# Kernel optimization log

Measured on AMD Instinct MI355X. Metric: run time of the kernel, lower is better.

The kernel has to match this reference:

```python
import jax, jax.numpy as jnp
import numpy as np

RES = 64
FDIM = 32
NMOD = 3
HID = 64
NCLS = 4
NFREQ = 6
IN_DIM = FDIM * NMOD + 3 * (2 * NFREQ + 1)  # 135


def trilinear_sample(grid, pts):
    """Torch F.grid_sample(mode='bilinear', padding_mode='zeros', align_corners=True).
    grid: [C, D, H, W]; pts: [M, 3] with (x, y, z) in [-1, 1], x indexes W, y->H, z->D.
    Returns [M, C]."""
    C, D, H, W = grid.shape
    x, y, z = pts[:, 0], pts[:, 1], pts[:, 2]
    ix = (x + 1.0) * 0.5 * (W - 1)
    iy = (y + 1.0) * 0.5 * (H - 1)
    iz = (z + 1.0) * 0.5 * (D - 1)
    ix0 = jnp.floor(ix); iy0 = jnp.floor(iy); iz0 = jnp.floor(iz)
    fx = ix - ix0; fy = iy - iy0; fz = iz - iz0
    ix0i = ix0.astype(jnp.int32); ix1i = ix0i + 1
    iy0i = iy0.astype(jnp.int32); iy1i = iy0i + 1
    iz0i = iz0.astype(jnp.int32); iz1i = iz0i + 1

    def corner(zc, yc, xc, w):
        valid = ((zc >= 0) & (zc < D) & (yc >= 0) & (yc < H) & (xc >= 0) & (xc < W))
        zcc = jnp.clip(zc, 0, D - 1)
        ycc = jnp.clip(yc, 0, H - 1)
        xcc = jnp.clip(xc, 0, W - 1)
        v = grid[:, zcc, ycc, xcc]  # [C, M]
        return v * (w * valid.astype(grid.dtype))

    wx0 = 1.0 - fx; wx1 = fx
    wy0 = 1.0 - fy; wy1 = fy
    wz0 = 1.0 - fz; wz1 = fz
    out = (corner(iz0i, iy0i, ix0i, wz0 * wy0 * wx0)
           + corner(iz0i, iy0i, ix1i, wz0 * wy0 * wx1)
           + corner(iz0i, iy1i, ix0i, wz0 * wy1 * wx0)
           + corner(iz0i, iy1i, ix1i, wz0 * wy1 * wx1)
           + corner(iz1i, iy0i, ix0i, wz1 * wy0 * wx0)
           + corner(iz1i, iy0i, ix1i, wz1 * wy0 * wx1)
           + corner(iz1i, iy1i, ix0i, wz1 * wy1 * wx0)
           + corner(iz1i, iy1i, ix1i, wz1 * wy1 * wx1))
    return out.T  # [M, C]


def positional_encoding(x):
    # gamma(p) = [p, sin(2^0 pi p), cos(2^0 pi p), ..., sin(2^(L-1) pi p), cos(2^(L-1) pi p)]
    freqs = 2.0 ** jnp.arange(NFREQ, dtype=x.dtype)  # [L]
    enc = [x]
    for i in range(NFREQ):
        a = jnp.pi * freqs[i] * x
        enc.append(jnp.sin(a))
        enc.append(jnp.cos(a))
    return jnp.concatenate(enc, axis=-1)  # [..., 3*(2L+1)]


def setup_inputs() -> dict:
    key = jax.random.key(0)
    ks = jax.random.split(key, 8)
    B, N = 4, 131072
    points = jax.random.uniform(ks[0], (B, N, 3), jnp.float32, -1.0, 1.0)
    grids = jax.random.normal(ks[1], (NMOD, FDIM, RES, RES, RES), jnp.float32) * 0.1

    def xavier(k, fan_in, fan_out):
        a = np.sqrt(6.0 / (fan_in + fan_out))
        return jax.random.uniform(k, (fan_in, fan_out), jnp.float32, -a, a)

    W0 = xavier(ks[2], IN_DIM, HID); b0 = jnp.zeros((HID,), jnp.float32)
    W1 = xavier(ks[3], HID, HID); b1 = jnp.zeros((HID,), jnp.float32)
    W2 = xavier(ks[4], HID, 1 + NCLS); b2 = jnp.zeros((1 + NCLS,), jnp.float32)
    return {"points": points, "grids": grids, "W0": W0, "b0": b0,
            "W1": W1, "b1": b1, "W2": W2, "b2": b2}


def reference(points, grids, W0, b0, W1, b1, W2, b2):
    B, N, _ = points.shape
    pts = points.reshape(B * N, 3)
    # fuse all 3 modalities: cat along feature dim, modality-major order
    feats = jax.vmap(lambda g: trilinear_sample(g, pts))(grids)  # [3, M, C]
    fused = jnp.transpose(feats, (1, 0, 2)).reshape(B * N, NMOD * FDIM)
    pe = positional_encoding(pts)  # [M, 39]
    h = jnp.concatenate([fused, pe], axis=-1)  # [M, 135]
    h = jax.nn.relu(h @ W0 + b0)
    h = jax.nn.relu(h @ W1 + b1)
    o = h @ W2 + b2  # [M, 1 + num_classes]
    density = jax.nn.softplus(o[..., 0]).reshape(B, N)
    seg_logits = o[..., 1:].reshape(B, N, NCLS)
    return density, seg_logits
```

## Files before the change

### kernel.cpp

```cpp
#include <hip/hip_runtime.h>
#include <hip/hip_bf16.h>
#include <hip/hip_fp16.h>
#include <math.h>

#define RESX 64
#define NVOX (RESX * RESX * RESX)
#define FDIM 32
#define NMOD 3
#define HID 64
#define NCLS 4
#define NFREQ 6
#define INDIM 135
#define TPB 64
#define XK 168
#define XSTR 65
#define MSTRIDE_B (NVOX * FDIM * 2)
#define NCELL 4096
#define NREP 16
#define NBT (NVOX / 128)
#define TRB (NMOD * NBT)
#define HISTB 2048
#define PACKB 15

typedef _Float16 f16x8 __attribute__((ext_vector_type(8)));
typedef float    f32x4 __attribute__((ext_vector_type(4)));

static __device__ __forceinline__ __half2 u2h(unsigned int u) {
    return __builtin_bit_cast(__half2, u);
}
static __device__ __forceinline__ unsigned int h2u(__half2 h) {
    return __builtin_bit_cast(unsigned int, h);
}

static __device__ __forceinline__ int cell_of(float px, float py, float pz) {
    int x0 = (int)floorf((px + 1.0f) * 0.5f * (RESX - 1));
    int y0 = (int)floorf((py + 1.0f) * 0.5f * (RESX - 1));
    int z0 = (int)floorf((pz + 1.0f) * 0.5f * (RESX - 1));
    x0 = min(max(x0, 0), RESX - 1);
    y0 = min(max(y0, 0), RESX - 1);
    z0 = min(max(z0, 0), RESX - 1);
    return ((z0 >> 2) << 8) | ((y0 >> 2) << 4) | (x0 >> 2);
}

#define W0PACK (5 * 4 * 64 * 8)
#define W1PACK (2 * 4 * 64 * 8)
#define W2PACK (2 * 64 * 8)

__global__ void pre_kernel(const float* __restrict__ g,
                           _Float16* __restrict__ gt,
                           const float* __restrict__ W0,
                           const float* __restrict__ W1,
                           const float* __restrict__ W2,
                           _Float16* __restrict__ wb,
                           const float* __restrict__ points,
                           unsigned int* __restrict__ hist, int M) {
    __shared__ float4 tile4[FDIM][33];
    const int bid = blockIdx.x;
    const int t   = threadIdx.x;
    if (bid < TRB) {
        const int m  = bid / NBT;
        const int v0 = (bid % NBT) * 128;
        const float4* g4 = reinterpret_cast<const float4*>(g);
#pragma unroll
        for (int k = 0; k < 4; ++k) {
            const int idx = k * 256 + t;
            const int c = idx >> 5, q = idx & 31;
            tile4[c][q] = g4[((size_t)(m * FDIM + c) * NVOX + v0) / 4 + q];
        }
        __syncthreads();
        uint4* gtu4 = reinterpret_cast<uint4*>(gt);
#pragma unroll
        for (int k = 0; k < 2; ++k) {
            const int idx = k * 256 + t;
            const int v = idx >> 2, q = idx & 3;
            const int vq = v >> 2, vr = v & 3;
            uint4 o;
            {
                const float a0 = reinterpret_cast<const float*>(&tile4[8 * q + 0][vq])[vr];
                const float a1 = reinterpret_cast<const float*>(&tile4[8 * q + 1][vq])[vr];
                const float a2 = reinterpret_cast<const float*>(&tile4[8 * q + 2][vq])[vr];
                const float a3 = reinterpret_cast<const float*>(&tile4[8 * q + 3][vq])[vr];
                const float a4 = reinterpret_cast<const float*>(&tile4[8 * q + 4][vq])[vr];
                const float a5 = reinterpret_cast<const float*>(&tile4[8 * q + 5][vq])[vr];
                const float a6 = reinterpret_cast<const float*>(&tile4[8 * q + 6][vq])[vr];
                const float a7 = reinterpret_cast<const float*>(&tile4[8 * q + 7][vq])[vr];
                o.x = h2u(__floats2half2_rn(a0, a1));
                o.y = h2u(__floats2half2_rn(a2, a3));
                o.z = h2u(__floats2half2_rn(a4, a5));
                o.w = h2u(__floats2half2_rn(a6, a7));
            }
            gtu4[(size_t)(m * NVOX + v0 + v) * 4 + q] = o;
        }
    } else if (bid < TRB + HISTB) {
        const int hb = bid - TRB;
        const int i  = hb * 256 + t;
        const int r  = hb & (NREP - 1);
        if (i < M) {
            const int c = cell_of(points[i * 3], points[i * 3 + 1], points[i * 3 + 2]);
            atomicAdd(&hist[r * NCELL + c], 1u);
        }
    } else {
        const int tt = (bid - TRB - HISTB) * 256 + t;
        const int NT = PACKB * 256;
        for (int idx = tt; idx < W0PACK; idx += NT) {
            const int j = idx & 7, l = (idx >> 3) & 63, nt = (idx >> 9) & 3, s = idx >> 11;
            const int k = 32 * s + (l >> 4) * 8 + j;
            const int o = 16 * nt + (l & 15);
            wb[idx] = (_Float16)((k < INDIM) ? W0[k * HID + o] : 0.0f);
        }
        for (int idx = tt; idx < W1PACK; idx += NT) {
            const int j = idx & 7, l = (idx >> 3) & 63, nt = (idx >> 9) & 3, s = idx >> 11;
            const int k = 32 * s + (l >> 4) * 8 + j;
            const int o = 16 * nt + (l & 15);
            wb[W0PACK + idx] = (_Float16)W1[k * HID + o];
        }
        for (int idx = tt; idx < W2PACK; idx += NT) {
            const int j = idx & 7, l = (idx >> 3) & 63, s = idx >> 9;
            const int k = 32 * s + (l >> 4) * 8 + j;
            const int o = l & 15;
            wb[W0PACK + W1PACK + idx] =
                (_Float16)((o < NCLS + 1) ? W2[k * (NCLS + 1) + o] : 0.0f);
        }
    }
}

__global__ void scan_rep_kernel(unsigned int* __restrict__ hist,
                                unsigned int* __restrict__ tot) {
    const int c = blockIdx.x * 256 + threadIdx.x;
    unsigned int run = 0;
#pragma unroll
    for (int r = 0; r < NREP; ++r) {
        const unsigned int v = hist[r * NCELL + c];
        hist[r * NCELL + c] = run;
        run += v;
    }
    tot[c] = run;
}

__global__ __launch_bounds__(1024) void scan_kernel(const unsigned int* __restrict__ tot,
                                                    unsigned int* __restrict__ cbase) {
    __shared__ unsigned int s[1024];
    const int t = threadIdx.x;
    unsigned int v[4];
#pragma unroll
    for (int j = 0; j < 4; ++j) v[j] = tot[4 * t + j];
    const unsigned int sum = v[0] + v[1] + v[2] + v[3];
    s[t] = sum;
    __syncthreads();
    for (int off = 1; off < 1024; off <<= 1) {
        const unsigned int x = (t >= off) ? s[t - off] : 0u;
        __syncthreads();
        s[t] += x;
        __syncthreads();
    }
    unsigned int excl = s[t] - sum;
#pragma unroll
    for (int j = 0; j < 4; ++j) { cbase[4 * t + j] = excl; excl += v[j]; }
}

__global__ void scatter_kernel(const float* __restrict__ points,
                               const unsigned int* __restrict__ cbase,
                               unsigned int* __restrict__ hist,
                               float4* __restrict__ pts4, int M) {
    const int i = blockIdx.x * 256 + threadIdx.x;
    if (i < M) {
        const float px = points[i * 3], py = points[i * 3 + 1], pz = points[i * 3 + 2];
        const int c = cell_of(px, py, pz);
        const int r = blockIdx.x & (NREP - 1);
        const unsigned int pos = cbase[c] + atomicAdd(&hist[r * NCELL + c], 1u);
        pts4[pos] = make_float4(px, py, pz, __int_as_float(i));
    }
}

template <bool SORT>
__global__ __launch_bounds__(256, 7) void fused_mfma_kernel(
    const float* __restrict__ points,
    const float4* __restrict__ pts4,
    const _Float16* __restrict__ gt,
    const _Float16* __restrict__ wb,
    const float* __restrict__ b0, const float* __restrict__ b1,
    const float* __restrict__ b2,
    float* __restrict__ density, float* __restrict__ seg) {
    __shared__ __align__(16) _Float16 Xs[TPB * XK];
    __shared__ __align__(16) uint4 PQ[TPB];
    const int tid = threadIdx.x;
    const int chunk = gridDim.x >> 3;
    const int sbid  = (blockIdx.x & 7) * chunk + (blockIdx.x >> 3);
    const int p0    = sbid * TPB;

    const int l = tid & 63;
    const int w = __builtin_amdgcn_readfirstlane(tid >> 6);

    float px = 0.0f, py = 0.0f, pz = 0.0f;
    int gp = 0;
    if (l < 16) {
        const int p  = w * 16 + l;
        const int sp = p0 + p;
        if (SORT) {
            const float4 q = pts4[sp];
            px = q.x; py = q.y; pz = q.z; gp = __float_as_int(q.w);
        } else {
            px = points[sp * 3]; py = points[sp * 3 + 1]; pz = points[sp * 3 + 2];
            gp = sp;
        }
        const float ix = (px + 1.0f) * 0.5f * (RESX - 1);
        const float iy = (py + 1.0f) * 0.5f * (RESX - 1);
        const float iz = (pz + 1.0f) * 0.5f * (RESX - 1);
        const float fx0 = floorf(ix), fy0 = floorf(iy), fz0 = floorf(iz);
        const float fx = ix - fx0, fy = iy - fy0, fz = iz - fz0;
        int x0 = (int)fx0, y0 = (int)fy0, z0 = (int)fz0;
        x0 = min(max(x0, 0), RESX - 1);
        y0 = min(max(y0, 0), RESX - 1);
        z0 = min(max(z0, 0), RESX - 1);
        const float wy0 = 1.0f - fy, wy1 = fy;
        const float wz0 = 1.0f - fz, wz1 = fz;
        const unsigned int b00 = (unsigned int)((z0 * 4096 + y0 * 64 + x0) * 64);
        unsigned int code =
            (unsigned int)__builtin_bit_cast(unsigned short, __float2half(fx));
        if (y0 < RESX - 1) code |= 0x10000u;
        if (z0 < RESX - 1) code |= 0x20000u;
        PQ[w * 16 + l] = make_uint4(b00, code,
                                    h2u(__floats2half2_rn(wz0 * wy0, wz0 * wy1)),
                                    h2u(__floats2half2_rn(wz1 * wy0, wz1 * wy1)));
    }

    {
        const int hw   = tid >> 5;
        const int lane = tid & 31;
        const int half = lane >> 4;
        const char* gbase = reinterpret_cast<const char*>(gt) + lane * 4;
        const __half2 one2 = __float2half2_rn(1.0f);
#pragma unroll
        for (int i = 0; i < 8; ++i) {
            const int p = hw * 8 + i;
            const uint4 q = PQ[p];
            const unsigned int dy = (q.y & 0x10000u) >> 4;
            const unsigned int dz = (q.y & 0x20000u) << 1;
            const unsigned int b00 = q.x;
            const unsigned int b01 = q.x + dy;
            const unsigned int b10 = q.x + dz;
            const unsigned int b11 = q.x + dy + dz;
            const __half fxh =
                __builtin_bit_cast(__half, (unsigned short)(q.y & 0xffffu));
            const __half2 fx2  = __half2half2(fxh);
            const __half2 wxh2 = half ? fx2 : __hsub2(one2, fx2);
            const __half2 wab = u2h(q.z);
            const __half2 wcd = u2h(q.w);
            const __half2 h00 = __hmul2(__low2half2(wab),  wxh2);
            const __half2 h01 = __hmul2(__high2half2(wab), wxh2);
            const __half2 h10 = __hmul2(__low2half2(wcd),  wxh2);
            const __half2 h11 = __hmul2(__high2half2(wcd), wxh2);
            unsigned int accu[NMOD];
#pragma unroll
            for (int m = 0; m < NMOD; ++m) {
                const char* gm = gbase + (size_t)m * MSTRIDE_B;
                const unsigned int u0 = *reinterpret_cast<const unsigned int*>(gm + b00);
                const unsigned int u1 = *reinterpret_cast<const unsigned int*>(gm + b01);
                const unsigned int u2 = *reinterpret_cast<const unsigned int*>(gm + b10);
                const unsigned int u3 = *reinterpret_cast<const unsigned int*>(gm + b11);
                __half2 a = __hmul2(h00, u2h(u0));
                a = __hfma2(h01, u2h(u1), a);
                a = __hfma2(h10, u2h(u2), a);
                a = __hfma2(h11, u2h(u3), a);
                accu[m] = h2u(a);
            }
#pragma unroll
            for (int m = 0; m < NMOD; ++m) {
                const unsigned int other = __shfl_xor(accu[m], 16, 64);
                const __half2 sum = __hadd2(u2h(accu[m]), u2h(other));
                if (lane < 16) {
                    *reinterpret_cast<unsigned int*>(
                        &Xs[p * XK + m * FDIM + 2 * (lane & 15)]) = h2u(sum);
                }
            }
        }
    }

    {
        const int src = l & 15;
        const float c0 = __shfl(px, src, 64);
        const float c1 = __shfl(py, src, 64);
        const float c2 = __shfl(pz, src, 64);
        const int pt  = w * 16 + src;
        const int gq2 = l >> 4;
        const float c3[3] = {c0, c1, c2};
        _Float16* xr = &Xs[pt * XK];
        if (gq2 == 3) {
            xr[96]  = (_Float16)c3[0];
            xr[97]  = (_Float16)c3[1];
            xr[98]  = (_Float16)c3[2];
            xr[135] = (_Float16)0.0f;
        }
        if (gq2 == 2) {
            unsigned int* xz = reinterpret_cast<unsigned int*>(&xr[136]);
#pragma unroll
            for (int k = 0; k < 12; ++k) xz[k] = 0u;
        }
        {
            const int f = gq2;
            const float hf = 0.5f * (float)(1 << f);
#pragma unroll
            for (int d = 0; d < 3; ++d) {
                const float r  = c3[d] * hf;
                const float rf = r - floorf(r);
                xr[99 + 6 * f + d]     = (_Float16)__builtin_amdgcn_sinf(rf);
                xr[99 + 6 * f + 3 + d] = (_Float16)__builtin_amdgcn_cosf(rf);
            }
        }
        if (gq2 < 2) {
            const int f = gq2 + 4;
            const float hf = 0.5f * (float)(1 << f);
#pragma unroll
            for (int d = 0; d < 3; ++d) {
                const float r  = c3[d] * hf;
                const float rf = r - floorf(r);
                xr[99 + 6 * f + d]     = (_Float16)__builtin_amdgcn_sinf(rf);
                xr[99 + 6 * f + 3 + d] = (_Float16)__builtin_amdgcn_cosf(rf);
            }
        }
    }

    const int col = l & 15;
    const int g   = l >> 4;

    f32x4 acc0[4];
#pragma unroll
    for (int nt = 0; nt < 4; ++nt) {
        const float bv = b0[nt * 16 + col];
        acc0[nt] = (f32x4){bv, bv, bv, bv};
    }
    {
        const _Float16* arow = &Xs[(w * 16 + col) * XK];
#pragma unroll
        for (int s = 0; s < 5; ++s) {
            const f16x8 af = *reinterpret_cast<const f16x8*>(arow + s * 32 + g * 8);
#pragma unroll
            for (int nt = 0; nt < 4; ++nt) {
                const f16x8 bfr = *reinterpret_cast<const f16x8*>(wb + (size_t)((s * 4 + nt) * 64 + l) * 8);
                acc0[nt] = __builtin_amdgcn_mfma_f32_16x16x32_f16(af, bfr, acc0[nt], 0, 0, 0);
            }
        }
    }
#pragma unroll
    for (int nt = 0; nt < 4; ++nt)
#pragma unroll
        for (int r = 0; r < 4; ++r) {
            Xs[(w * 16 + g * 4 + r) * XK + 96 + nt * 16 + col] =
                (_Float16)fmaxf(acc0[nt][r], 0.0f);
        }

    f32x4 acc1[4];
#pragma unroll
    for (int nt = 0; nt < 4; ++nt) {
        const float bv = b1[nt * 16 + col];
        acc1[nt] = (f32x4){bv, bv, bv, bv};
    }
    {
        const _Float16* arow = &Xs[(w * 16 + col) * XK + 96];
        const _Float16* wb1  = wb + W0PACK;
#pragma unroll
        for (int s = 0; s < 2; ++s) {
            const f16x8 af = *reinterpret_cast<const f16x8*>(arow + s * 32 + g * 8);
#pragma unroll
            for (int nt = 0; nt < 4; ++nt) {
                const f16x8 bfr = *reinterpret_cast<const f16x8*>(wb1 + (size_t)((s * 4 + nt) * 64 + l) * 8);
                acc1[nt] = __builtin_amdgcn_mfma_f32_16x16x32_f16(af, bfr, acc1[nt], 0, 0, 0);
            }
        }
    }
#pragma unroll
    for (int nt = 0; nt < 4; ++nt)
#pragma unroll
        for (int r = 0; r < 4; ++r) {
            Xs[(w * 16 + g * 4 + r) * XK + nt * 16 + col] =
                (_Float16)fmaxf(acc1[nt][r], 0.0f);
        }

    f32x4 acc2;
    {
        const float bv = (col < NCLS + 1) ? b2[col] : 0.0f;
        acc2 = (f32x4){bv, bv, bv, bv};
        const _Float16* arow = &Xs[(w * 16 + col) * XK];
        const _Float16* wb2  = wb + W0PACK + W1PACK;
#pragma unroll
        for (int s = 0; s < 2; ++s) {
            const f16x8 af  = *reinterpret_cast<const f16x8*>(arow + s * 32 + g * 8);
            const f16x8 bfr = *reinterpret_cast<const f16x8*>(wb2 + (size_t)(s * 64 + l) * 8);
            acc2 = __builtin_amdgcn_mfma_f32_16x16x32_f16(af, bfr, acc2, 0, 0, 0);
        }
    }
    if (col < NCLS + 1) {
        float* osr = reinterpret_cast<float*>(&Xs[0]);
#pragma unroll
        for (int r = 0; r < 4; ++r) {
            const int row = w * 16 + g * 4 + r;
            osr[(row * XK + 128) / 2 + col] = acc2[r];
        }
    }

    if (l < 16) {
        const int row = w * 16 + l;
        const float* osr = reinterpret_cast<const float*>(&Xs[0]) + (row * XK + 128) / 2;
        const float4 o0123 = *reinterpret_cast<const float4*>(osr);
        const float o4 = osr[4];
        const float e  = __builtin_amdgcn_exp2f(fabsf(o0123.x) * -1.44269504f);
        const float sp = fmaxf(o0123.x, 0.0f) + 0.69314718f * __builtin_amdgcn_logf(1.0f + e);
        density[gp] = sp;
        reinterpret_cast<float4*>(seg)[gp] = make_float4(o0123.y, o0123.z, o0123.w, o4);
    }
}

__global__ __launch_bounds__(256, 4) void fused_nerf_fallback(
    const float* __restrict__ points,
    const float* __restrict__ grids,
    const float* __restrict__ W0, const float* __restrict__ b0,
    const float* __restrict__ W1, const float* __restrict__ b1,
    const float* __restrict__ W2, const float* __restrict__ b2,
    float* __restrict__ density, float* __restrict__ seg) {
    __shared__ float xT[INDIM + 1][XSTR];
    const int tid = threadIdx.x;
    const int p0  = blockIdx.x * TPB;
    {
        const int hw   = tid >> 5;
        const int lane = tid & 31;
        for (int i = 0; i < TPB / 8; ++i) {
            const int p  = hw * (TPB / 8) + i;
            const int gp = p0 + p;
            const float px = points[gp * 3 + 0];
            const float py = points[gp * 3 + 1];
            const float pz = points[gp * 3 + 2];
            const float ix = (px + 1.0f) * 0.5f * (RESX - 1);
            const float iy = (py + 1.0f) * 0.5f * (RESX - 1);
            const float iz = (pz + 1.0f) * 0.5f * (RESX - 1);
            const float fx0 = floorf(ix), fy0 = floorf(iy), fz0 = floorf(iz);
            const float fx = ix - fx0, fy = iy - fy0, fz = iz - fz0;
            int ix0 = (int)fx0, iy0 = (int)fy0, iz0 = (int)fz0;
            ix0 = min(max(ix0, 0), RESX - 1);
            iy0 = min(max(iy0, 0), RESX - 1);
            iz0 = min(max(iz0, 0), RESX - 1);
            const int ix1 = min(ix0 + 1, RESX - 1);
            const int iy1 = min(iy0 + 1, RESX - 1);
            const int iz1 = min(iz0 + 1, RESX - 1);
            const float wx1 = fx, wx0 = 1.0f - fx;
            const float wy1 = fy, wy0 = 1.0f - fy;
            const float wz1 = fz, wz0 = 1.0f - fz;
            const int vz0 = iz0 * 4096, vz1 = iz1 * 4096;
            const int vy0 = iy0 * 64,   vy1 = iy1 * 64;
            const int v000 = vz0 + vy0 + ix0, v001 = vz0 + vy0 + ix1;
            const int v010 = vz0 + vy1 + ix0, v011 = vz0 + vy1 + ix1;
            const int v100 = vz1 + vy0 + ix0, v101 = vz1 + vy0 + ix1;
            const int v110 = vz1 + vy1 + ix0, v111 = vz1 + vy1 + ix1;
            const float w000 = wz0 * wy0 * wx0, w001 = wz0 * wy0 * wx1;
            const float w010 = wz0 * wy1 * wx0, w011 = wz0 * wy1 * wx1;
            const float w100 = wz1 * wy0 * wx0, w101 = wz1 * wy0 * wx1;
            const float w110 = wz1 * wy1 * wx0, w111 = wz1 * wy1 * wx1;
#pragma unroll
            for (int m = 0; m < NMOD; ++m) {
                const float* gb = grids + (size_t)(m * FDIM + lane) * NVOX;
                float acc;
                acc = w000 * gb[v000];
                acc = fmaf(w001, gb[v001], acc);
                acc = fmaf(w010, gb[v010], acc);
                acc = fmaf(w011, gb[v011], acc);
                acc = fmaf(w100, gb[v100], acc);
                acc = fmaf(w101, gb[v101], acc);
                acc = fmaf(w110, gb[v110], acc);
                acc = fmaf(w111, gb[v111], acc);
                xT[m * FDIM + lane][p] = acc;
            }
        }
    }
    {
        const int p  = tid & 63;
        const int gq = tid >> 6;
        const int gp = p0 + p;
        float c3[3];
        c3[0] = points[gp * 3 + 0];
        c3[1] = points[gp * 3 + 1];
        c3[2] = points[gp * 3 + 2];
        if (gq == 3) {
#pragma unroll
            for (int d = 0; d < 3; ++d) xT[96 + d][p] = c3[d];
        }
#pragma unroll
        for (int f = 0; f < NFREQ; ++f) {
            if ((f & 3) != gq) continue;
            const float fr = (float)(1 << f);
#pragma unroll
            for (int d = 0; d < 3; ++d) {
                const float a = 3.14159274101257324f * fr * c3[d];
                xT[99 + 6 * f + d][p]     = sinf(a);
                xT[99 + 6 * f + 3 + d][p] = cosf(a);
            }
        }
    }
    __syncthreads();
    const int pl = tid & 63;
    const int wv = __builtin_amdgcn_readfirstlane(tid >> 6);
    const int gp = p0 + pl;
    float acc[16];
#pragma unroll
    for (int j = 0; j < 16; ++j) acc[j] = b0[wv * 16 + j];
    for (int k = 0; k < INDIM; ++k) {
        const float xk = xT[k][pl];
        const float* wr = W0 + k * HID + wv * 16;
#pragma unroll
        for (int j = 0; j < 16; ++j) acc[j] = fmaf(xk, wr[j], acc[j]);
    }
#pragma unroll
    for (int j = 0; j < 16; ++j) acc[j] = fmaxf(acc[j], 0.0f);
    __syncthreads();
#pragma unroll
    for (int j = 0; j < 16; ++j) xT[wv * 16 + j][pl] = acc[j];
    __syncthreads();
    float acc1[16];
#pragma unroll
    for (int j = 0; j < 16; ++j) acc1[j] = b1[wv * 16 + j];
    for (int k = 0; k < HID; ++k) {
        const float xk = xT[k][pl];
        const float* wr = W1 + k * HID + wv * 16;
#pragma unroll
        for (int j = 0; j < 16; ++j) acc1[j] = fmaf(xk, wr[j], acc1[j]);
    }
#pragma unroll
    for (int j = 0; j < 16; ++j) acc1[j] = fmaxf(acc1[j], 0.0f);
    __syncthreads();
#pragma unroll
    for (int j = 0; j < 16; ++j) xT[wv * 16 + j][pl] = acc1[j];
    __syncthreads();
    if (wv == 0) {
        float o[5];
#pragma unroll
        for (int j = 0; j < 5; ++j) o[j] = b2[j];
        for (int k = 0; k < HID; ++k) {
            const float xk = xT[k][pl];
            const float* wr = W2 + k * (1 + NCLS);
#pragma unroll
            for (int j = 0; j < 5; ++j) o[j] = fmaf(xk, wr[j], o[j]);
        }
        const float d = fmaxf(o[0], 0.0f) + log1pf(expf(-fabsf(o[0])));
        density[gp] = d;
        reinterpret_cast<float4*>(seg)[gp] = make_float4(o[1], o[2], o[3], o[4]);
    }
}

extern "C" void kernel_launch(void* const* d_in, const int* in_sizes, int n_in,
                              void* d_out, int out_size, void* d_ws, size_t ws_size,
                              hipStream_t stream) {
    const float* points = (const float*)d_in[0];
    const float* grids  = (const float*)d_in[1];
    const float* W0     = (const float*)d_in[2];
    const float* b0     = (const float*)d_in[3];
    const float* W1     = (const float*)d_in[4];
    const float* b1     = (const float*)d_in[5];
    const float* W2     = (const float*)d_in[6];
    const float* b2     = (const float*)d_in[7];

    const int M = in_sizes[0] / 3;
    float* density = (float*)d_out;
    float* seg     = density + M;

    const size_t gt_b   = (size_t)NMOD * NVOX * FDIM * sizeof(_Float16);
    const size_t wb_b   = 32768;
    const size_t hist_b = (size_t)NREP * NCELL * sizeof(unsigned int);
    const size_t tot_b  = NCELL * sizeof(unsigned int);
    const size_t cb_b   = NCELL * sizeof(unsigned int);
    const size_t pts_b  = (size_t)M * sizeof(float4);
    const int nblk = M / TPB;

    if (ws_size >= gt_b + wb_b + hist_b + tot_b + cb_b + pts_b) {
        char* p = (char*)d_ws;
        _Float16*     gt    = (_Float16*)p;      p += gt_b;
        _Float16*     wbp   = (_Float16*)p;      p += wb_b;
        unsigned int* hist  = (unsigned int*)p;  p += hist_b;
        unsigned int* tot   = (unsigned int*)p;  p += tot_b;
        unsigned int* cbase = (unsigned int*)p;  p += cb_b;
        float4*       pts4  = (float4*)p;

        hipMemsetAsync(hist, 0, hist_b, stream);
        pre_kernel<<<TRB + HISTB + PACKB, 256, 0, stream>>>(
            grids, gt, W0, W1, W2, wbp, points, hist, M);
        scan_rep_kernel<<<NCELL / 256, 256, 0, stream>>>(hist, tot);
        scan_kernel<<<1, 1024, 0, stream>>>(tot, cbase);
        scatter_kernel<<<(M + 255) / 256, 256, 0, stream>>>(points, cbase, hist, pts4, M);
        fused_mfma_kernel<true><<<nblk, 256, 0, stream>>>(
            points, pts4, gt, wbp, b0, b1, b2, density, seg);
    } else if (ws_size >= gt_b + wb_b) {
        char* p = (char*)d_ws;
        _Float16* gt  = (_Float16*)p;  p += gt_b;
        _Float16* wbp = (_Float16*)p;
        pre_kernel<<<TRB + HISTB + PACKB, 256, 0, stream>>>(
            grids, gt, W0, W1, W2, wbp, points, (unsigned int*)nullptr, 0);
        fused_mfma_kernel<false><<<nblk, 256, 0, stream>>>(
            points, (const float4*)nullptr, gt, wbp, b0, b1, b2, density, seg);
    } else {
        fused_nerf_fallback<<<nblk, 256, 0, stream>>>(
            points, grids, W0, b0, W1, b1, W2, b2, density, seg);
    }
}
```

Baseline: 150.3 us.

## Replace global scan with atomic cell allocation and batch grid gathers

Drops the single-block prefix-scan kernel. Each cell now claims its output range with an atomicAdd on a global cursor and adds that base into its per-replica offsets, so the scatter kernel no longer reads cbase. Cells are therefore laid out in nondeterministic rather than spatial order, which may weaken the locality the sort is meant to give. Separately, the trilinear gather loop now issues all 96 grid loads for its 8 points before doing any arithmetic, to expose more memory-level parallelism at the cost of higher register pressure under launch_bounds(256,7).

Result: slower. 338.4 us (+125.2%).

```diff
diff --git a/kernel.cpp b/kernel.cpp
--- a/kernel.cpp
+++ b/kernel.cpp
@@ -125,7 +125,7 @@
 }
 
 __global__ void scan_rep_kernel(unsigned int* __restrict__ hist,
-                                unsigned int* __restrict__ tot) {
+                                unsigned int* __restrict__ cursor) {
     const int c = blockIdx.x * 256 + threadIdx.x;
     unsigned int run = 0;
 #pragma unroll
@@ -134,32 +134,12 @@
         hist[r * NCELL + c] = run;
         run += v;
     }
-    tot[c] = run;
-}
-
-__global__ __launch_bounds__(1024) void scan_kernel(const unsigned int* __restrict__ tot,
-                                                    unsigned int* __restrict__ cbase) {
-    __shared__ unsigned int s[1024];
-    const int t = threadIdx.x;
-    unsigned int v[4];
-#pragma unroll
-    for (int j = 0; j < 4; ++j) v[j] = tot[4 * t + j];
-    const unsigned int sum = v[0] + v[1] + v[2] + v[3];
-    s[t] = sum;
-    __syncthreads();
-    for (int off = 1; off < 1024; off <<= 1) {
-        const unsigned int x = (t >= off) ? s[t - off] : 0u;
-        __syncthreads();
-        s[t] += x;
-        __syncthreads();
-    }
-    unsigned int excl = s[t] - sum;
-#pragma unroll
-    for (int j = 0; j < 4; ++j) { cbase[4 * t + j] = excl; excl += v[j]; }
+    const unsigned int base = atomicAdd(cursor, run);
+#pragma unroll
+    for (int r = 0; r < NREP; ++r) hist[r * NCELL + c] += base;
 }
 
 __global__ void scatter_kernel(const float* __restrict__ points,
-                               const unsigned int* __restrict__ cbase,
                                unsigned int* __restrict__ hist,
                                float4* __restrict__ pts4, int M) {
     const int i = blockIdx.x * 256 + threadIdx.x;
@@ -167,7 +147,7 @@
         const float px = points[i * 3], py = points[i * 3 + 1], pz = points[i * 3 + 2];
         const int c = cell_of(px, py, pz);
         const int r = blockIdx.x & (NREP - 1);
-        const unsigned int pos = cbase[c] + atomicAdd(&hist[r * NCELL + c], 1u);
+        const unsigned int pos = atomicAdd(&hist[r * NCELL + c], 1u);
         pts4[pos] = make_float4(px, py, pz, __int_as_float(i));
     }
 }
@@ -230,22 +210,39 @@
         const int half = lane >> 4;
         const char* gbase = reinterpret_cast<const char*>(gt) + lane * 4;
         const __half2 one2 = __float2half2_rn(1.0f);
+
+        uint4 q[8];
+#pragma unroll
+        for (int i = 0; i < 8; ++i) q[i] = PQ[hw * 8 + i];
+
+        unsigned int u[8][12];
+#pragma unroll
+        for (int i = 0; i < 8; ++i) {
+            const unsigned int dy  = (q[i].y & 0x10000u) >> 4;
+            const unsigned int dz  = (q[i].y & 0x20000u) << 1;
+            const unsigned int b00 = q[i].x;
+            const unsigned int b01 = b00 + dy;
+            const unsigned int b10 = b00 + dz;
+            const unsigned int b11 = b00 + dy + dz;
+#pragma unroll
+            for (int m = 0; m < NMOD; ++m) {
+                const char* gm = gbase + (size_t)m * MSTRIDE_B;
+                u[i][m * 4 + 0] = *reinterpret_cast<const unsigned int*>(gm + b00);
+                u[i][m * 4 + 1] = *reinterpret_cast<const unsigned int*>(gm + b01);
+                u[i][m * 4 + 2] = *reinterpret_cast<const unsigned int*>(gm + b10);
+                u[i][m * 4 + 3] = *reinterpret_cast<const unsigned int*>(gm + b11);
+            }
+        }
+
 #pragma unroll
         for (int i = 0; i < 8; ++i) {
             const int p = hw * 8 + i;
-            const uint4 q = PQ[p];
-            const unsigned int dy = (q.y & 0x10000u) >> 4;
-            const unsigned int dz = (q.y & 0x20000u) << 1;
-            const unsigned int b00 = q.x;
-            const unsigned int b01 = q.x + dy;
-            const unsigned int b10 = q.x + dz;
-            const unsigned int b11 = q.x + dy + dz;
             const __half fxh =
-                __builtin_bit_cast(__half, (unsigned short)(q.y & 0xffffu));
+                __builtin_bit_cast(__half, (unsigned short)(q[i].y & 0xffffu));
             const __half2 fx2  = __half2half2(fxh);
             const __half2 wxh2 = half ? fx2 : __hsub2(one2, fx2);
-            const __half2 wab = u2h(q.z);
-            const __half2 wcd = u2h(q.w);
+            const __half2 wab = u2h(q[i].z);
+            const __half2 wcd = u2h(q[i].w);
             const __half2 h00 = __hmul2(__low2half2(wab),  wxh2);
             const __half2 h01 = __hmul2(__high2half2(wab), wxh2);
             const __half2 h10 = __hmul2(__low2half2(wcd),  wxh2);
@@ -253,15 +250,10 @@
             unsigned int accu[NMOD];
 #pragma unroll
             for (int m = 0; m < NMOD; ++m) {
-                const char* gm = gbase + (size_t)m * MSTRIDE_B;
-                const unsigned int u0 = *reinterpret_cast<const unsigned int*>(gm + b00);
-                const unsigned int u1 = *reinterpret_cast<const unsigned int*>(gm + b01);
-                const unsigned int u2 = *reinterpret_cast<const unsigned int*>(gm + b10);
-                const unsigned int u3 = *reinterpret_cast<const unsigned int*>(gm + b11);
-                __half2 a = __hmul2(h00, u2h(u0));
-                a = __hfma2(h01, u2h(u1), a);
-                a = __hfma2(h10, u2h(u2), a);
-                a = __hfma2(h11, u2h(u3), a);
+                __half2 a = __hmul2(h00, u2h(u[i][m * 4 + 0]));
+                a = __hfma2(h01, u2h(u[i][m * 4 + 1]), a);
+                a = __hfma2(h10, u2h(u[i][m * 4 + 2]), a);
+                a = __hfma2(h11, u2h(u[i][m * 4 + 3]), a);
                 accu[m] = h2u(a);
             }
 #pragma unroll
@@ -563,26 +555,23 @@
     const size_t gt_b   = (size_t)NMOD * NVOX * FDIM * sizeof(_Float16);
     const size_t wb_b   = 32768;
     const size_t hist_b = (size_t)NREP * NCELL * sizeof(unsigned int);
-    const size_t tot_b  = NCELL * sizeof(unsigned int);
-    const size_t cb_b   = NCELL * sizeof(unsigned int);
+    const size_t cur_b  = 16;
     const size_t pts_b  = (size_t)M * sizeof(float4);
     const int nblk = M / TPB;
 
-    if (ws_size >= gt_b + wb_b + hist_b + tot_b + cb_b + pts_b) {
+    if (ws_size >= gt_b + wb_b + hist_b + cur_b + pts_b) {
         char* p = (char*)d_ws;
-        _Float16*     gt    = (_Float16*)p;      p += gt_b;
-        _Float16*     wbp   = (_Float16*)p;      p += wb_b;
-        unsigned int* hist  = (unsigned int*)p;  p += hist_b;
-        unsigned int* tot   = (unsigned int*)p;  p += tot_b;
-        unsigned int* cbase = (unsigned int*)p;  p += cb_b;
-        float4*       pts4  = (float4*)p;
-
-        hipMemsetAsync(hist, 0, hist_b, stream);
+        _Float16*     gt     = (_Float16*)p;      p += gt_b;
+        _Float16*     wbp    = (_Float16*)p;      p += wb_b;
+        unsigned int* hist   = (unsigned int*)p;  p += hist_b;
+        unsigned int* cursor = (unsigned int*)p;  p += cur_b;
+        float4*       pts4   = (float4*)p;
+
+        hipMemsetAsync(hist, 0, hist_b + cur_b, stream);
         pre_kernel<<<TRB + HISTB + PACKB, 256, 0, stream>>>(
             grids, gt, W0, W1, W2, wbp, points, hist, M);
-        scan_rep_kernel<<<NCELL / 256, 256, 0, stream>>>(hist, tot);
-        scan_kernel<<<1, 1024, 0, stream>>>(tot, cbase);
-        scatter_kernel<<<(M + 255) / 256, 256, 0, stream>>>(points, cbase, hist, pts4, M);
+        scan_rep_kernel<<<NCELL / 256, 256, 0, stream>>>(hist, cursor);
+        scatter_kernel<<<(M + 255) / 256, 256, 0, stream>>>(points, hist, pts4, M);
         fused_mfma_kernel<true><<<nblk, 256, 0, stream>>>(
             points, pts4, gt, wbp, b0, b1, b2, density, seg);
     } else if (ws_size >= gt_b + wb_b) {
```
